# Performance work log

Measured on AMD Instinct MI355X. Metric: run time of the kernel, lower is better.

The kernel has to match this reference:

```python
import jax, jax.numpy as jnp
import numpy as np

N, E, G = 50000, 800000, 512
F, DE, DG = 64, 16, 32
H, HEADS, C, L, NC = 128, 4, 32, 3, 1
EPS = 1e-5


def _bn(x, g, b, m, v):
    # eval-mode BatchNorm1d with running stats
    return (x - m) / jnp.sqrt(v + EPS) * g + b


def setup_inputs():
    key = jax.random.key(0)
    ks = jax.random.split(key, 24)

    def bn_params(k, d):
        k1, k2, k3, k4 = jax.random.split(k, 4)
        return (1.0 + 0.1 * jax.random.normal(k1, (d,), jnp.float32),
                0.1 * jax.random.normal(k2, (d,), jnp.float32),
                0.1 * jax.random.normal(k3, (d,), jnp.float32),
                jax.random.uniform(k4, (d,), jnp.float32, 0.5, 1.5))

    sc = lambda k, sh, fan: jax.random.normal(k, sh, jnp.float32) / np.float32(np.sqrt(fan))
    inp = {}
    inp['x'] = jax.random.normal(ks[0], (N, F), jnp.float32)
    inp['edge_attr'] = jax.random.normal(ks[1], (E, DE), jnp.float32)
    inp['global_features'] = jax.random.normal(ks[2], (G, DG), jnp.float32)
    inp['edge_index'] = jax.random.randint(ks[3], (2, E), 0, N)
    inp['batch'] = jnp.sort(jax.random.randint(ks[4], (N,), 0, G))
    inp['node_w'] = sc(ks[5], (F, H), F); inp['node_b'] = jnp.zeros((H,), jnp.float32)
    inp['node_bn_g'], inp['node_bn_b'], inp['node_bn_m'], inp['node_bn_v'] = bn_params(ks[6], H)
    inp['edge_w'] = sc(ks[7], (DE, H), DE); inp['edge_b'] = jnp.zeros((H,), jnp.float32)
    inp['glob_w'] = sc(ks[8], (DG, H), DG); inp['glob_b'] = jnp.zeros((H,), jnp.float32)
    inp['glob_bn_g'], inp['glob_bn_b'], inp['glob_bn_m'], inp['glob_bn_v'] = bn_params(ks[9], H)
    inp['gat_lin'] = sc(ks[10], (L, H, HEADS * C), H)
    inp['gat_asrc'] = sc(ks[11], (L, HEADS, C), C)
    inp['gat_adst'] = sc(ks[12], (L, HEADS, C), C)
    inp['gat_bias'] = jnp.zeros((L, H), jnp.float32)
    bg, bb, bm, bv = zip(*[bn_params(jax.random.fold_in(ks[13], i), H) for i in range(L)])
    inp['bn_g'] = jnp.stack(bg); inp['bn_b'] = jnp.stack(bb)
    inp['bn_m'] = jnp.stack(bm); inp['bn_v'] = jnp.stack(bv)
    inp['lin1_w'] = sc(ks[14], (3 * H, H), 3 * H); inp['lin1_b'] = jnp.zeros((H,), jnp.float32)
    inp['lin2_w'] = sc(ks[15], (H, NC), H); inp['lin2_b'] = jnp.zeros((NC,), jnp.float32)
    return inp


def reference(x, edge_attr, global_features, edge_index, batch, node_w, node_b, node_bn_g, node_bn_b, node_bn_m, node_bn_v, edge_w, edge_b, glob_w, glob_b, glob_bn_g, glob_bn_b, glob_bn_m, glob_bn_v, gat_lin, gat_asrc, gat_adst, gat_bias, bn_g, bn_b, bn_m, bn_v, lin1_w, lin1_b, lin2_w, lin2_b):
    n = x.shape[0]
    h = jax.nn.relu(_bn(x @ node_w + node_b, node_bn_g, node_bn_b, node_bn_m, node_bn_v))
    _ = jax.nn.relu(edge_attr @ edge_w + edge_b)  # edge encoder: computed but unused by GATConv, as in source
    # add self loops (PyG GATConv default)
    loops = jnp.arange(n)
    src = jnp.concatenate([edge_index[0], loops])
    dst = jnp.concatenate([edge_index[1], loops])
    for i in range(L):
        identity = h
        hh = (h @ gat_lin[i]).reshape(n, HEADS, C)
        a_src = jnp.einsum('nhc,hc->nh', hh, gat_asrc[i])
        a_dst = jnp.einsum('nhc,hc->nh', hh, gat_adst[i])
        e = jax.nn.leaky_relu(a_src[src] + a_dst[dst], 0.2)  # [E+n, HEADS]
        e_max = jax.ops.segment_max(e, dst, num_segments=n)
        ee = jnp.exp(e - e_max[dst])
        den = jax.ops.segment_sum(ee, dst, num_segments=n)
        alpha = ee / (den[dst] + 1e-16)
        out = jax.ops.segment_sum(hh[src] * alpha[..., None], dst, num_segments=n)
        out = out.reshape(n, HEADS * C) + gat_bias[i]
        out = jax.nn.relu(_bn(out, bn_g[i], bn_b[i], bn_m[i], bn_v[i]))
        h = out + identity  # residual: dims always match (HEADS*C == H)
    g = global_features.shape[0]
    cnt = jax.ops.segment_sum(jnp.ones((n,), h.dtype), batch, num_segments=g)
    x_mean = jax.ops.segment_sum(h, batch, num_segments=g) / jnp.maximum(cnt, 1.0)[:, None]
    x_max = jax.ops.segment_max(h, batch, num_segments=g)
    x_max = jnp.where(jnp.isfinite(x_max), x_max, 0.0)  # guard rare empty graphs
    gfeat = jax.nn.relu(_bn(global_features @ glob_w + glob_b, glob_bn_g, glob_bn_b, glob_bn_m, glob_bn_v))
    z = jnp.concatenate([x_mean, x_max, gfeat], axis=1)
    z = jax.nn.relu(z @ lin1_w + lin1_b)
    return z @ lin2_w + lin2_b
```

## Files before the change

### kernel.cpp

```cpp
#include <hip/hip_runtime.h>
#include <hip/hip_bf16.h>

typedef unsigned short u16;
typedef unsigned int   u32;
typedef unsigned long long u64;

#define HD 128
#define FD 64
#define EPS 1e-5f

using bf16x8 = __attribute__((ext_vector_type(8))) short;
using f32x4  = __attribute__((ext_vector_type(4))) float;

__device__ __forceinline__ float b2f(u16 v) { return __uint_as_float(((u32)v) << 16); }
__device__ __forceinline__ u16 f2b(float f) {
    u32 u = __float_as_uint(f);
    return (u16)((u + 0x7FFF + ((u >> 16) & 1)) >> 16);
}
__device__ __forceinline__ float lo16(u32 u) { return __uint_as_float(u << 16); }
__device__ __forceinline__ float hi16(u32 u) { return __uint_as_float(u & 0xFFFF0000u); }

__device__ __forceinline__ bf16x8 pack8(const float* p) {
    bf16x8 r;
    #pragma unroll
    for (int j = 0; j < 8; j++) r[j] = (short)f2b(p[j]);
    return r;
}

__global__ __launch_bounds__(256) void k_hist(const int* __restrict__ dst, int* __restrict__ cnt, int E) {
    int e = blockIdx.x * 256 + threadIdx.x;
    if (e < E) atomicAdd(&cnt[dst[e]], 1);
}

__global__ __launch_bounds__(256) void k_scanA(const int* __restrict__ cnt, int* __restrict__ rowptr,
                                               int* __restrict__ bsum, int N) {
    __shared__ int s[256];
    int tid = threadIdx.x;
    int i = blockIdx.x * 256 + tid;
    s[tid] = (i < N) ? cnt[i] : 0;
    __syncthreads();
    for (int off = 1; off < 256; off <<= 1) {
        int t = (tid >= off) ? s[tid - off] : 0;
        __syncthreads();
        s[tid] += t;
        __syncthreads();
    }
    if (i < N) rowptr[i + 1] = s[tid];
    if (tid == 255) bsum[blockIdx.x] = s[255];
}

__global__ __launch_bounds__(256) void k_scanB(int* __restrict__ bsum, int SB) {
    __shared__ int s[256];
    int tid = threadIdx.x;
    s[tid] = (tid < SB) ? bsum[tid] : 0;
    __syncthreads();
    for (int off = 1; off < 256; off <<= 1) {
        int t = (tid >= off) ? s[tid - off] : 0;
        __syncthreads();
        s[tid] += t;
        __syncthreads();
    }
    if (tid < SB) bsum[tid] = s[tid];
}

__global__ __launch_bounds__(256) void k_scanC(int* __restrict__ rowptr, const int* __restrict__ bsum, int N) {
    int i = blockIdx.x * 256 + threadIdx.x;
    if (i == 0) rowptr[0] = 0;
    if (i < N) {
        int b = i >> 8;
        if (b > 0) rowptr[i + 1] += bsum[b - 1];
    }
}

__global__ __launch_bounds__(256) void k_gbound(const int* __restrict__ batch, int* __restrict__ gs, int N, int G) {
    int i = blockIdx.x * 256 + threadIdx.x;
    if (i < N) {
        int b = batch[i];
        if (i == 0) { for (int g = 0; g <= b; g++) gs[g] = 0; }
        else {
            int pb = batch[i - 1];
            for (int g = pb + 1; g <= b; g++) gs[g] = i;
        }
        if (i == N - 1) { for (int g = b + 1; g <= G; g++) gs[g] = N; }
    }
}

__global__ __launch_bounds__(256) void k_binA(
    const int* __restrict__ src, const int* __restrict__ dst, const int* __restrict__ rowptr,
    int* __restrict__ bcur, u64* __restrict__ binned, int E, int bsh, int NB, int numTiles) {
    __shared__ u32 os[4096], od[4096];
    __shared__ int hist[256], obase[256], ofs[256], gpos[256];
    int tid = threadIdx.x;
    for (int t = blockIdx.x; t < numTiles; t += gridDim.x) {
        int base = t * 4096;
        int cnt = E - base; if (cnt > 4096) cnt = 4096;
        hist[tid] = 0;
        __syncthreads();
        u32 rs[16], rd[16];
        #pragma unroll
        for (int r = 0; r < 16; r++) {
            int li = r * 256 + tid;
            if (li < cnt) {
                rs[r] = src[base + li];
                rd[r] = dst[base + li];
                atomicAdd(&hist[rd[r] >> bsh], 1);
            }
        }
        __syncthreads();
        if (tid < 64) {
            int h0 = hist[4 * tid], h1 = hist[4 * tid + 1];
            int h2 = hist[4 * tid + 2], h3 = hist[4 * tid + 3];
            int s01 = h0 + h1;
            int loc = s01 + h2 + h3;
            int inc = loc;
            #pragma unroll
            for (int off = 1; off < 64; off <<= 1) {
                int tv = __shfl_up(inc, off);
                if (tid >= off) inc += tv;
            }
            int excl = inc - loc;
            obase[4 * tid] = excl;           ofs[4 * tid] = excl;
            obase[4 * tid + 1] = excl + h0;  ofs[4 * tid + 1] = excl + h0;
            obase[4 * tid + 2] = excl + s01; ofs[4 * tid + 2] = excl + s01;
            obase[4 * tid + 3] = excl + s01 + h2; ofs[4 * tid + 3] = excl + s01 + h2;
        }
        __syncthreads();
        #pragma unroll
        for (int r = 0; r < 16; r++) {
            int li = r * 256 + tid;
            if (li < cnt) {
                int b = rd[r] >> bsh;
                int posn = atomicAdd(&ofs[b], 1);
                os[posn] = rs[r];
                od[posn] = rd[r];
            }
        }
        __syncthreads();
        if (tid < NB && hist[tid] > 0)
            gpos[tid] = rowptr[tid << bsh] + atomicAdd(&bcur[tid], hist[tid]);
        __syncthreads();
        for (int li = tid; li < cnt; li += 256) {
            u32 d = od[li];
            int b = d >> bsh;
            binned[(size_t)gpos[b] + (li - obase[b])] = ((u64)d << 32) | os[li];
        }
        __syncthreads();
    }
}

__global__ __launch_bounds__(256) void k_binB(
    const u64* __restrict__ binned, const int* __restrict__ rowptr,
    int* __restrict__ colidx, int N, int bsh) {
    __shared__ int lofs[1024];
    int b = blockIdx.x;
    int n0 = b << bsh;
    int n1 = (b + 1) << bsh; if (n1 > N) n1 = N;
    int nb = 1 << bsh;
    for (int i = threadIdx.x; i < nb; i += 256) lofs[i] = 0;
    __syncthreads();
    int r0 = rowptr[n0], r1 = rowptr[n1];
    for (int i = r0 + threadIdx.x; i < r1; i += 256) {
        u64 pk = binned[i];
        u32 d = (u32)(pk >> 32), s = (u32)pk;
        int slot = atomicAdd(&lofs[d - n0], 1);
        colidx[rowptr[d] + slot] = (int)s;
    }
}

__global__ __launch_bounds__(256) void k_wprep(const float* __restrict__ node_w, const float* __restrict__ gat_lin,
                                               u16* __restrict__ wf_node, u16* __restrict__ wf_gat) {
    int y = blockIdx.y;
    const float* src; u16* dst; int K;
    if (y == 0) { src = node_w; dst = wf_node; K = FD; }
    else { src = gat_lin + (size_t)(y - 1) * HD * HD; dst = wf_gat + (size_t)(y - 1) * HD * HD; K = HD; }
    int KT = K >> 5;
    int total = K * HD;
    for (int f = blockIdx.x * 256 + threadIdx.x; f < total; f += gridDim.x * 256) {
        int j = f & 7;
        int lane = (f >> 3) & 63;
        int t = f >> 9;
        int kt = t % KT;
        int ct = t / KT;
        int k = kt * 32 + (lane >> 4) * 8 + j;
        int col = ct * 16 + (lane & 15);
        dst[f] = f2b(src[k * HD + col]);
    }
}

__global__ __launch_bounds__(256) void k_node_mfma(
    const float* __restrict__ x, const u16* __restrict__ wf, const float* __restrict__ bias,
    const float* __restrict__ g, const float* __restrict__ bb, const float* __restrict__ m,
    const float* __restrict__ v, u16* __restrict__ h, int N) {
    int wv = threadIdx.x >> 6, lane = threadIdx.x & 63;
    int rowbase = blockIdx.x * 64 + wv * 16;
    if (rowbase >= N) return;
    int n16 = lane & 15, quad = lane >> 4;
    int arow = min(rowbase + n16, N - 1);
    f32x4 acc[8] = {};
    #pragma unroll
    for (int kt = 0; kt < 2; kt++) {
        bf16x8 a = pack8(x + (size_t)arow * FD + kt * 32 + quad * 8);
        #pragma unroll
        for (int ct = 0; ct < 8; ct++) {
            bf16x8 b = *(const bf16x8*)(wf + ((size_t)(ct * 2 + kt) * 64 + lane) * 8);
            acc[ct] = __builtin_amdgcn_mfma_f32_16x16x32_bf16(a, b, acc[ct], 0, 0, 0);
        }
    }
    #pragma unroll
    for (int ct = 0; ct < 8; ct++) {
        int col = ct * 16 + n16;
        float sc = g[col] * rsqrtf(v[col] + EPS);
        float bi = (bias[col] - m[col]) * sc + bb[col];
        #pragma unroll
        for (int reg = 0; reg < 4; reg++) {
            int row = rowbase + quad * 4 + reg;
            if (row < N) h[(size_t)row * HD + col] = f2b(fmaxf(acc[ct][reg] * sc + bi, 0.f));
        }
    }
}

__global__ __launch_bounds__(256) void k_gat_mfma(
    const u16* __restrict__ h, const u16* __restrict__ wf,
    const float* __restrict__ asrcw, const float* __restrict__ adstw,
    u16* __restrict__ hh, float* __restrict__ a_src, float* __restrict__ a_dst, int N) {
    int wv = threadIdx.x >> 6, lane = threadIdx.x & 63;
    int rowbase = blockIdx.x * 64 + wv * 16;
    if (rowbase >= N) return;
    int n16 = lane & 15, quad = lane >> 4;
    int arow = min(rowbase + n16, N - 1);
    f32x4 acc[8] = {};
    #pragma unroll
    for (int kt = 0; kt < 4; kt++) {
        bf16x8 a = *(const bf16x8*)(h + (size_t)arow * HD + kt * 32 + quad * 8);
        #pragma unroll
        for (int ct = 0; ct < 8; ct++) {
            bf16x8 b = *(const bf16x8*)(wf + ((size_t)(ct * 4 + kt) * 64 + lane) * 8);
            acc[ct] = __builtin_amdgcn_mfma_f32_16x16x32_bf16(a, b, acc[ct], 0, 0, 0);
        }
    }
    float asw[8], adw[8];
    #pragma unroll
    for (int ct = 0; ct < 8; ct++) {
        asw[ct] = asrcw[ct * 16 + n16];
        adw[ct] = adstw[ct * 16 + n16];
    }
    float ps[4][4], pd[4][4];
    #pragma unroll
    for (int hd = 0; hd < 4; hd++)
        #pragma unroll
        for (int reg = 0; reg < 4; reg++) {
            ps[hd][reg] = acc[2 * hd][reg] * asw[2 * hd] + acc[2 * hd + 1][reg] * asw[2 * hd + 1];
            pd[hd][reg] = acc[2 * hd][reg] * adw[2 * hd] + acc[2 * hd + 1][reg] * adw[2 * hd + 1];
        }
    #pragma unroll
    for (int msk = 1; msk < 16; msk <<= 1) {
        #pragma unroll
        for (int hd = 0; hd < 4; hd++)
            #pragma unroll
            for (int reg = 0; reg < 4; reg++) {
                ps[hd][reg] += __shfl_xor(ps[hd][reg], msk);
                pd[hd][reg] += __shfl_xor(pd[hd][reg], msk);
            }
    }
    #pragma unroll
    for (int reg = 0; reg < 4; reg++) {
        int row = rowbase + quad * 4 + reg;
        if (row < N) {
            #pragma unroll
            for (int ct = 0; ct < 8; ct++)
                hh[(size_t)row * HD + ct * 16 + n16] = f2b(acc[ct][reg]);
            if (n16 < 4) {
                float ws = 0.f, wd = 0.f;
                #pragma unroll
                for (int hd = 0; hd < 4; hd++)
                    if (n16 == hd) { ws = ps[hd][reg]; wd = pd[hd][reg]; }
                a_src[row * 4 + n16] = ws;
                a_dst[row * 4 + n16] = wd;
            }
        }
    }
}

__global__ __launch_bounds__(256) void k_agg(
    u16* __restrict__ h, const u32* __restrict__ hh32,
    const float* __restrict__ a_src, const float* __restrict__ a_dst,
    const int* __restrict__ rowptr, const int* __restrict__ colidx,
    const float* __restrict__ bias, const float* __restrict__ bng, const float* __restrict__ bnb,
    const float* __restrict__ bnm, const float* __restrict__ bnv, int N) {
    __shared__ int   sL[4][64];
    __shared__ __align__(16) float eeL[4][64][4];
    int wv = threadIdx.x >> 6, lane = threadIdx.x & 63;
    int node = blockIdx.x * 4 + wv;
    if (node >= N) return;
    int head = lane >> 4;
    const float4* as4p = (const float4*)a_src;
    float4 ad4 = ((const float4*)a_dst)[node];
    float adh = (head == 0) ? ad4.x : (head == 1) ? ad4.y : (head == 2) ? ad4.z : ad4.w;
    float ash = a_src[node * 4 + head];
    float e = ash + adh;
    e = (e > 0.f) ? e : 0.2f * e;
    float ee = __expf(e);
    float den = ee;
    u32 hv = hh32[(size_t)node * 64 + lane];
    float acc0 = ee * lo16(hv), acc1 = ee * hi16(hv);
    int beg = rowptr[node], end = rowptr[node + 1];
    for (int base = beg; base < end; base += 64) {
        int cnt = end - base; if (cnt > 64) cnt = 64;
        int s = 0;
        float4 e4 = {0.f, 0.f, 0.f, 0.f};
        if (lane < cnt) {
            s = colidx[base + lane];
            float4 as4 = as4p[s];
            float t0 = as4.x + ad4.x, t1 = as4.y + ad4.y, t2 = as4.z + ad4.z, t3 = as4.w + ad4.w;
            t0 = (t0 > 0.f) ? t0 : 0.2f * t0; t1 = (t1 > 0.f) ? t1 : 0.2f * t1;
            t2 = (t2 > 0.f) ? t2 : 0.2f * t2; t3 = (t3 > 0.f) ? t3 : 0.2f * t3;
            e4.x = __expf(t0); e4.y = __expf(t1); e4.z = __expf(t2); e4.w = __expf(t3);
        }
        sL[wv][lane] = s;
        ((float4*)eeL[wv][lane])[0] = e4;
        int j = 0;
        for (; j + 8 <= cnt; j += 8) {
            u32 hv2[8]; float w[8];
            #pragma unroll
            for (int q = 0; q < 8; q++) {
                int sj = sL[wv][j + q];
                w[q] = eeL[wv][j + q][head];
                hv2[q] = hh32[(size_t)sj * 64 + lane];
            }
            #pragma unroll
            for (int q = 0; q < 8; q++) {
                den += w[q];
                acc0 += w[q] * lo16(hv2[q]);
                acc1 += w[q] * hi16(hv2[q]);
            }
        }
        for (; j < cnt; j++) {
            int sj = sL[wv][j];
            float w = eeL[wv][j][head];
            u32 hv2 = hh32[(size_t)sj * 64 + lane];
            den += w;
            acc0 += w * lo16(hv2);
            acc1 += w * hi16(hv2);
        }
    }
    float inv = 1.0f / (den + 1e-16f);
    int c0 = lane * 2, c1 = c0 + 1;
    float o0 = acc0 * inv, o1 = acc1 * inv;
    float sc0 = bng[c0] * rsqrtf(bnv[c0] + EPS);
    float sc1 = bng[c1] * rsqrtf(bnv[c1] + EPS);
    o0 = (o0 + bias[c0] - bnm[c0]) * sc0 + bnb[c0];
    o1 = (o1 + bias[c1] - bnm[c1]) * sc1 + bnb[c1];
    o0 = fmaxf(o0, 0.f); o1 = fmaxf(o1, 0.f);
    u32 idv = ((const u32*)h)[(size_t)node * 64 + lane];
    o0 += lo16(idv); o1 += hi16(idv);
    ((u32*)h)[(size_t)node * 64 + lane] = ((u32)f2b(o1) << 16) | f2b(o0);
}

__global__ __launch_bounds__(256) void k_pool(
    const u16* __restrict__ h, const int* __restrict__ gs,
    const float* __restrict__ gf, const float* __restrict__ glob_w, const float* __restrict__ glob_b,
    const float* __restrict__ gbg, const float* __restrict__ gbb,
    const float* __restrict__ gbm, const float* __restrict__ gbv,
    float* __restrict__ z, int N, int G) {
    __shared__ float s0L[4][64], s1L[4][64], m0L[4][64], m1L[4][64];
    int g = blockIdx.x, tid = threadIdx.x;
    int wv = tid >> 6, lane = tid & 63;
    int beg = gs[g], end = gs[g + 1];
    const u32* h32 = (const u32*)h;
    float s0 = 0.f, s1 = 0.f, m0 = -3.4e38f, m1 = -3.4e38f;
    for (int r = beg + wv; r < end; r += 4) {
        u32 pk = h32[(size_t)r * 64 + lane];
        float v0 = lo16(pk), v1 = hi16(pk);
        s0 += v0; s1 += v1;
        m0 = fmaxf(m0, v0); m1 = fmaxf(m1, v1);
    }
    s0L[wv][lane] = s0; s1L[wv][lane] = s1;
    m0L[wv][lane] = m0; m1L[wv][lane] = m1;
    __syncthreads();
    if (tid < 64) {
        float a0 = s0L[0][lane] + s0L[1][lane] + s0L[2][lane] + s0L[3][lane];
        float a1 = s1L[0][lane] + s1L[1][lane] + s1L[2][lane] + s1L[3][lane];
        float x0 = fmaxf(fmaxf(m0L[0][lane], m0L[1][lane]), fmaxf(m0L[2][lane], m0L[3][lane]));
        float x1 = fmaxf(fmaxf(m1L[0][lane], m1L[1][lane]), fmaxf(m1L[2][lane], m1L[3][lane]));
        int cnt = end - beg;
        float inv = 1.0f / (float)(cnt > 0 ? cnt : 1);
        if (cnt == 0) { x0 = 0.f; x1 = 0.f; }
        ((float2*)(z + (size_t)g * 384))[lane] = make_float2(a0 * inv, a1 * inv);
        ((float2*)(z + (size_t)g * 384 + 128))[lane] = make_float2(x0, x1);
    } else if (tid >= 128) {
        int c = tid - 128;
        float acc = glob_b[c];
        #pragma unroll 8
        for (int k = 0; k < 32; k++) acc += gf[g * 32 + k] * glob_w[k * HD + c];
        float sc = gbg[c] * rsqrtf(gbv[c] + EPS);
        acc = (acc - gbm[c]) * sc + gbb[c];
        z[(size_t)g * 384 + 256 + c] = fmaxf(acc, 0.f);
    }
}

__global__ __launch_bounds__(256) void k_lin(
    const float* __restrict__ z, const float* __restrict__ W1, const float* __restrict__ b1,
    const float* __restrict__ W2, const float* __restrict__ b2, float* __restrict__ out, int G) {
    __shared__ float zL[8][384];
    __shared__ float Wc[64][128];
    __shared__ float red[8][128];
    int tid = threadIdx.x;
    int g0 = blockIdx.x * 8;
    int c = tid & 127, half = tid >> 7;
    for (int i = tid; i < 8 * 384; i += 256) {
        int gi = i / 384, kk = i % 384;
        zL[gi][kk] = (g0 + gi < G) ? z[(size_t)(g0 + gi) * 384 + kk] : 0.f;
    }
    float acc0 = 0.f, acc1 = 0.f, acc2 = 0.f, acc3 = 0.f;
    int gb = half * 4;
    for (int ch = 0; ch < 6; ch++) {
        __syncthreads();
        for (int i4 = tid; i4 < 2048; i4 += 256) {
            int flat = i4 * 4;
            int k = flat >> 7, cc = flat & 127;
            *(float4*)&Wc[k][cc] = *(const float4*)&W1[(size_t)(ch * 64 + k) * HD + cc];
        }
        __syncthreads();
        int kb = ch * 64;
        #pragma unroll 4
        for (int k = 0; k < 64; k++) {
            float w = Wc[k][c];
            acc0 += zL[gb + 0][kb + k] * w;
            acc1 += zL[gb + 1][kb + k] * w;
            acc2 += zL[gb + 2][kb + k] * w;
            acc3 += zL[gb + 3][kb + k] * w;
        }
    }
    float b1c = b1[c], w2c = W2[c];
    __syncthreads();
    red[gb + 0][c] = fmaxf(acc0 + b1c, 0.f) * w2c;
    red[gb + 1][c] = fmaxf(acc1 + b1c, 0.f) * w2c;
    red[gb + 2][c] = fmaxf(acc2 + b1c, 0.f) * w2c;
    red[gb + 3][c] = fmaxf(acc3 + b1c, 0.f) * w2c;
    __syncthreads();
    int gr = tid >> 5, l32 = tid & 31;
    float v = red[gr][l32] + red[gr][l32 + 32] + red[gr][l32 + 64] + red[gr][l32 + 96];
    #pragma unroll
    for (int m = 1; m < 32; m <<= 1) v += __shfl_xor(v, m, 32);
    if (l32 == 0 && g0 + gr < G) out[g0 + gr] = v + b2[0];
}

extern "C" void kernel_launch(void* const* d_in, const int* in_sizes, int n_in,
                              void* d_out, int out_size, void* d_ws, size_t ws_size,
                              hipStream_t stream) {
    (void)n_in; (void)out_size; (void)ws_size;
    const float* x        = (const float*)d_in[0];
    const float* gfeat    = (const float*)d_in[2];
    const int*   ei       = (const int*)d_in[3];
    const int*   batch    = (const int*)d_in[4];
    const float* node_w   = (const float*)d_in[5];
    const float* node_b   = (const float*)d_in[6];
    const float* nbg      = (const float*)d_in[7];
    const float* nbb      = (const float*)d_in[8];
    const float* nbm      = (const float*)d_in[9];
    const float* nbv      = (const float*)d_in[10];
    const float* glob_w   = (const float*)d_in[13];
    const float* glob_b   = (const float*)d_in[14];
    const float* gbg      = (const float*)d_in[15];
    const float* gbb      = (const float*)d_in[16];
    const float* gbm      = (const float*)d_in[17];
    const float* gbv      = (const float*)d_in[18];
    const float* gat_lin  = (const float*)d_in[19];
    const float* gat_asrc = (const float*)d_in[20];
    const float* gat_adst = (const float*)d_in[21];
    const float* gat_bias = (const float*)d_in[22];
    const float* bn_g     = (const float*)d_in[23];
    const float* bn_b     = (const float*)d_in[24];
    const float* bn_m     = (const float*)d_in[25];
    const float* bn_v     = (const float*)d_in[26];
    const float* lin1_w   = (const float*)d_in[27];
    const float* lin1_b   = (const float*)d_in[28];
    const float* lin2_w   = (const float*)d_in[29];
    const float* lin2_b   = (const float*)d_in[30];

    const int N = in_sizes[0] / FD;
    const int E = in_sizes[3] / 2;
    const int G = in_sizes[2] / 32;
    const int* srcp = ei;
    const int* dstp = ei + E;

    int bsh = 8;
    while (((N + (1 << bsh) - 1) >> bsh) > 256) bsh++;
    const int NB = (N + (1 << bsh) - 1) >> bsh;

    char* p = (char*)d_ws;
    auto alloc = [&](size_t bytes) -> char* {
        char* r = p;
        p += (bytes + 255) & ~(size_t)255;
        return r;
    };
    u16*   h       = (u16*)alloc((size_t)N * HD * 2);
    u16*   hh      = (u16*)alloc((size_t)N * HD * 2);
    float* a_src   = (float*)alloc((size_t)N * 4 * 4);
    float* a_dst   = (float*)alloc((size_t)N * 4 * 4);
    int*   rowptr  = (int*)alloc((size_t)(N + 1) * 4);
    char*  zbase   = p;
    int*   cnt     = (int*)alloc((size_t)N * 4);
    int*   bcur    = (int*)alloc(256 * 4);
    size_t zbytes  = (size_t)(p - zbase);
    int*   bsum    = (int*)alloc(256 * 4);
    int*   colidx  = (int*)alloc((size_t)E * 4);
    u64*   binned  = (u64*)alloc((size_t)E * 8);
    u16*   wf_node = (u16*)alloc((size_t)FD * HD * 2);
    u16*   wf_gat  = (u16*)alloc((size_t)3 * HD * HD * 2);
    float* z       = (float*)alloc((size_t)G * 384 * 4);
    int*   gs      = (int*)alloc((size_t)(G + 1) * 4);

    hipMemsetAsync(zbase, 0, zbytes, stream);

    k_wprep<<<dim3(32, 4), 256, 0, stream>>>(node_w, gat_lin, wf_node, wf_gat);

    int eb = (E + 255) / 256;
    int SB = (N + 255) / 256;
    k_hist<<<eb, 256, 0, stream>>>(dstp, cnt, E);
    k_scanA<<<SB, 256, 0, stream>>>(cnt, rowptr, bsum, N);
    k_scanB<<<1, 256, 0, stream>>>(bsum, SB);
    k_scanC<<<SB, 256, 0, stream>>>(rowptr, bsum, N);
    k_gbound<<<SB, 256, 0, stream>>>(batch, gs, N, G);

    int numTiles = (E + 4095) / 4096;
    int binAGrid = numTiles < 512 ? numTiles : 512;
    k_binA<<<binAGrid, 256, 0, stream>>>(srcp, dstp, rowptr, bcur, binned, E, bsh, NB, numTiles);
    k_binB<<<NB, 256, 0, stream>>>(binned, rowptr, colidx, N, bsh);

    k_node_mfma<<<(N + 63) / 64, 256, 0, stream>>>(x, wf_node, node_b, nbg, nbb, nbm, nbv, h, N);

    for (int i = 0; i < 3; i++) {
        k_gat_mfma<<<(N + 63) / 64, 256, 0, stream>>>(
            h, wf_gat + (size_t)i * HD * HD,
            gat_asrc + i * HD, gat_adst + i * HD,
            hh, a_src, a_dst, N);
        k_agg<<<(N + 3) / 4, 256, 0, stream>>>(
            h, (const u32*)hh, a_src, a_dst, rowptr, colidx,
            gat_bias + i * HD, bn_g + i * HD, bn_b + i * HD, bn_m + i * HD, bn_v + i * HD, N);
    }

    k_pool<<<G, 256, 0, stream>>>(h, gs, gfeat, glob_w, glob_b, gbg, gbb, gbm, gbv, z, N, G);
    k_lin<<<(G + 7) / 8, 256, 0, stream>>>(z, lin1_w, lin1_b, lin2_w, lin2_b, (float*)d_out, G);
}
```

Measured before the change: 424.8 us.

## Fuse CSR build, node embedding and readout into fewer kernels with chained scan

Merges weight prep, graph-boundary computation and workspace zeroing into one prep kernel. Fuses the degree histogram into edge binning, which now writes into fixed-capacity per-bucket arenas and runs concurrently with the node-embedding MFMA blocks. Replaces the three-pass scan and second binning pass with a single decoupled chained-scan kernel that also scatters column indices. Fuses pooling with the final MLP. This cuts launch overhead and intermediate traffic, but assumes no bucket exceeds CAP edges and relies on cross-block spin-waits.

After: 706.1 us. +66.2%, slower.

```diff
diff --git a/kernel.cpp b/kernel.cpp
--- a/kernel.cpp
+++ b/kernel.cpp
@@ -8,6 +8,8 @@
 #define HD 128
 #define FD 64
 #define EPS 1e-5f
+#define BSH 8
+#define CAP 8192
 
 using bf16x8 = __attribute__((ext_vector_type(8))) short;
 using f32x4  = __attribute__((ext_vector_type(4))) float;
@@ -20,90 +22,74 @@
 __device__ __forceinline__ float lo16(u32 u) { return __uint_as_float(u << 16); }
 __device__ __forceinline__ float hi16(u32 u) { return __uint_as_float(u & 0xFFFF0000u); }
 
-__device__ __forceinline__ bf16x8 pack8(const float* p) {
-    bf16x8 r;
-    #pragma unroll
-    for (int j = 0; j < 8; j++) r[j] = (short)f2b(p[j]);
-    return r;
-}
-
-__global__ __launch_bounds__(256) void k_hist(const int* __restrict__ dst, int* __restrict__ cnt, int E) {
-    int e = blockIdx.x * 256 + threadIdx.x;
-    if (e < E) atomicAdd(&cnt[dst[e]], 1);
-}
-
-__global__ __launch_bounds__(256) void k_scanA(const int* __restrict__ cnt, int* __restrict__ rowptr,
-                                               int* __restrict__ bsum, int N) {
-    __shared__ int s[256];
+__global__ __launch_bounds__(256) void k_prep(
+    const float* __restrict__ node_w, const float* __restrict__ gat_lin,
+    u16* __restrict__ wf_node, u16* __restrict__ wf_gat,
+    const int* __restrict__ batch, int* __restrict__ gs,
+    int* __restrict__ zbase, int zn, int N, int G) {
+    int y = blockIdx.y;
     int tid = threadIdx.x;
-    int i = blockIdx.x * 256 + tid;
-    s[tid] = (i < N) ? cnt[i] : 0;
-    __syncthreads();
-    for (int off = 1; off < 256; off <<= 1) {
-        int t = (tid >= off) ? s[tid - off] : 0;
-        __syncthreads();
-        s[tid] += t;
-        __syncthreads();
-    }
-    if (i < N) rowptr[i + 1] = s[tid];
-    if (tid == 255) bsum[blockIdx.x] = s[255];
-}
-
-__global__ __launch_bounds__(256) void k_scanB(int* __restrict__ bsum, int SB) {
-    __shared__ int s[256];
+    if (y < 4) {
+        const float* src; u16* dst; int K;
+        if (y == 0) { src = node_w; dst = wf_node; K = FD; }
+        else { src = gat_lin + (size_t)(y - 1) * HD * HD; dst = wf_gat + (size_t)(y - 1) * HD * HD; K = HD; }
+        int KT = K >> 5;
+        int total = K * HD;
+        for (int f = blockIdx.x * 256 + tid; f < total; f += gridDim.x * 256) {
+            int j = f & 7;
+            int lane = (f >> 3) & 63;
+            int t = f >> 9;
+            int kt = t % KT;
+            int ct = t / KT;
+            int k = kt * 32 + (lane >> 4) * 8 + j;
+            int col = ct * 16 + (lane & 15);
+            dst[f] = f2b(src[k * HD + col]);
+        }
+    } else if (y == 4) {
+        int i = blockIdx.x * 256 + tid;
+        if (i < N) {
+            int b = batch[i];
+            if (i == 0) { for (int g = 0; g <= b; g++) gs[g] = 0; }
+            else {
+                int pb = batch[i - 1];
+                for (int g = pb + 1; g <= b; g++) gs[g] = i;
+            }
+            if (i == N - 1) { for (int g = b + 1; g <= G; g++) gs[g] = N; }
+        }
+    } else {
+        for (int i = blockIdx.x * 256 + tid; i < zn; i += gridDim.x * 256) zbase[i] = 0;
+    }
+}
+
+__global__ __launch_bounds__(256) void k_binA_node(
+    const int* __restrict__ src, const int* __restrict__ dst,
+    int* __restrict__ cnt, int* __restrict__ bcur, u64* __restrict__ arena,
+    const float* __restrict__ x, const u16* __restrict__ wf, const float* __restrict__ bias,
+    const float* __restrict__ g, const float* __restrict__ bb, const float* __restrict__ m,
+    const float* __restrict__ v, u16* __restrict__ h,
+    int E, int NB, int numTiles, int N) {
+    __shared__ __align__(16) char smem[4096 * 8 + 4 * 256 * 4];
     int tid = threadIdx.x;
-    s[tid] = (tid < SB) ? bsum[tid] : 0;
-    __syncthreads();
-    for (int off = 1; off < 256; off <<= 1) {
-        int t = (tid >= off) ? s[tid - off] : 0;
-        __syncthreads();
-        s[tid] += t;
-        __syncthreads();
-    }
-    if (tid < SB) bsum[tid] = s[tid];
-}
-
-__global__ __launch_bounds__(256) void k_scanC(int* __restrict__ rowptr, const int* __restrict__ bsum, int N) {
-    int i = blockIdx.x * 256 + threadIdx.x;
-    if (i == 0) rowptr[0] = 0;
-    if (i < N) {
-        int b = i >> 8;
-        if (b > 0) rowptr[i + 1] += bsum[b - 1];
-    }
-}
-
-__global__ __launch_bounds__(256) void k_gbound(const int* __restrict__ batch, int* __restrict__ gs, int N, int G) {
-    int i = blockIdx.x * 256 + threadIdx.x;
-    if (i < N) {
-        int b = batch[i];
-        if (i == 0) { for (int g = 0; g <= b; g++) gs[g] = 0; }
-        else {
-            int pb = batch[i - 1];
-            for (int g = pb + 1; g <= b; g++) gs[g] = i;
-        }
-        if (i == N - 1) { for (int g = b + 1; g <= G; g++) gs[g] = N; }
-    }
-}
-
-__global__ __launch_bounds__(256) void k_binA(
-    const int* __restrict__ src, const int* __restrict__ dst, const int* __restrict__ rowptr,
-    int* __restrict__ bcur, u64* __restrict__ binned, int E, int bsh, int NB, int numTiles) {
-    __shared__ u32 os[4096], od[4096];
-    __shared__ int hist[256], obase[256], ofs[256], gpos[256];
-    int tid = threadIdx.x;
-    for (int t = blockIdx.x; t < numTiles; t += gridDim.x) {
-        int base = t * 4096;
-        int cnt = E - base; if (cnt > 4096) cnt = 4096;
+    if ((int)blockIdx.x < numTiles) {
+        u32* os   = (u32*)smem;
+        u32* od   = os + 4096;
+        int* hist = (int*)(od + 4096);
+        int* obas = hist + 256;
+        int* ofs  = obas + 256;
+        int* gpos = ofs + 256;
+        int base = blockIdx.x * 4096;
+        int cntE = E - base; if (cntE > 4096) cntE = 4096;
         hist[tid] = 0;
         __syncthreads();
         u32 rs[16], rd[16];
         #pragma unroll
         for (int r = 0; r < 16; r++) {
             int li = r * 256 + tid;
-            if (li < cnt) {
+            if (li < cntE) {
                 rs[r] = src[base + li];
                 rd[r] = dst[base + li];
-                atomicAdd(&hist[rd[r] >> bsh], 1);
+                atomicAdd(&hist[rd[r] >> BSH], 1);
+                atomicAdd(&cnt[rd[r]], 1);
             }
         }
         __syncthreads();
@@ -119,17 +105,17 @@
                 if (tid >= off) inc += tv;
             }
             int excl = inc - loc;
-            obase[4 * tid] = excl;           ofs[4 * tid] = excl;
-            obase[4 * tid + 1] = excl + h0;  ofs[4 * tid + 1] = excl + h0;
-            obase[4 * tid + 2] = excl + s01; ofs[4 * tid + 2] = excl + s01;
-            obase[4 * tid + 3] = excl + s01 + h2; ofs[4 * tid + 3] = excl + s01 + h2;
+            obas[4 * tid] = excl;                 ofs[4 * tid] = excl;
+            obas[4 * tid + 1] = excl + h0;        ofs[4 * tid + 1] = excl + h0;
+            obas[4 * tid + 2] = excl + s01;       ofs[4 * tid + 2] = excl + s01;
+            obas[4 * tid + 3] = excl + s01 + h2;  ofs[4 * tid + 3] = excl + s01 + h2;
         }
         __syncthreads();
         #pragma unroll
         for (int r = 0; r < 16; r++) {
             int li = r * 256 + tid;
-            if (li < cnt) {
-                int b = rd[r] >> bsh;
+            if (li < cntE) {
+                int b = rd[r] >> BSH;
                 int posn = atomicAdd(&ofs[b], 1);
                 os[posn] = rs[r];
                 od[posn] = rd[r];
@@ -137,85 +123,107 @@
         }
         __syncthreads();
         if (tid < NB && hist[tid] > 0)
-            gpos[tid] = rowptr[tid << bsh] + atomicAdd(&bcur[tid], hist[tid]);
-        __syncthreads();
-        for (int li = tid; li < cnt; li += 256) {
+            gpos[tid] = atomicAdd(&bcur[tid], hist[tid]);
+        __syncthreads();
+        for (int li = tid; li < cntE; li += 256) {
             u32 d = od[li];
-            int b = d >> bsh;
-            binned[(size_t)gpos[b] + (li - obase[b])] = ((u64)d << 32) | os[li];
-        }
-        __syncthreads();
-    }
-}
-
-__global__ __launch_bounds__(256) void k_binB(
-    const u64* __restrict__ binned, const int* __restrict__ rowptr,
-    int* __restrict__ colidx, int N, int bsh) {
-    __shared__ int lofs[1024];
-    int b = blockIdx.x;
-    int n0 = b << bsh;
-    int n1 = (b + 1) << bsh; if (n1 > N) n1 = N;
-    int nb = 1 << bsh;
-    for (int i = threadIdx.x; i < nb; i += 256) lofs[i] = 0;
-    __syncthreads();
-    int r0 = rowptr[n0], r1 = rowptr[n1];
-    for (int i = r0 + threadIdx.x; i < r1; i += 256) {
-        u64 pk = binned[i];
-        u32 d = (u32)(pk >> 32), s = (u32)pk;
+            int b = d >> BSH;
+            int p = gpos[b] + (li - obas[b]);
+            if (p < CAP) arena[(size_t)b * CAP + p] = ((u64)d << 32) | os[li];
+        }
+    } else {
+        int nb = blockIdx.x - numTiles;
+        int wv = tid >> 6, lane = tid & 63;
+        int rowbase = nb * 64 + wv * 16;
+        if (rowbase >= N) return;
+        int n16 = lane & 15, quad = lane >> 4;
+        int arow = min(rowbase + n16, N - 1);
+        f32x4 acc[8] = {};
+        #pragma unroll
+        for (int kt = 0; kt < 2; kt++) {
+            const float4* xp = (const float4*)(x + (size_t)arow * FD + kt * 32 + quad * 8);
+            float4 a0 = xp[0], a1 = xp[1];
+            bf16x8 a;
+            a[0] = (short)f2b(a0.x); a[1] = (short)f2b(a0.y);
+            a[2] = (short)f2b(a0.z); a[3] = (short)f2b(a0.w);
+            a[4] = (short)f2b(a1.x); a[5] = (short)f2b(a1.y);
+            a[6] = (short)f2b(a1.z); a[7] = (short)f2b(a1.w);
+            #pragma unroll
+            for (int ct = 0; ct < 8; ct++) {
+                bf16x8 b = *(const bf16x8*)(wf + ((size_t)(ct * 2 + kt) * 64 + lane) * 8);
+                acc[ct] = __builtin_amdgcn_mfma_f32_16x16x32_bf16(a, b, acc[ct], 0, 0, 0);
+            }
+        }
+        #pragma unroll
+        for (int ct = 0; ct < 8; ct++) {
+            int col = ct * 16 + n16;
+            float sc = g[col] * rsqrtf(v[col] + EPS);
+            float bi = (bias[col] - m[col]) * sc + bb[col];
+            #pragma unroll
+            for (int reg = 0; reg < 4; reg++) {
+                int row = rowbase + quad * 4 + reg;
+                if (row < N) h[(size_t)row * HD + col] = f2b(fmaxf(acc[ct][reg] * sc + bi, 0.f));
+            }
+        }
+    }
+}
+
+__global__ __launch_bounds__(256) void k_scanB2(
+    const int* __restrict__ cnt, int* __restrict__ rowptr,
+    const u64* __restrict__ arena, const int* __restrict__ bcur,
+    int* __restrict__ colidx, int* __restrict__ ready, int* __restrict__ bval, int N) {
+    __shared__ int rowL[256], lofs[256], cL[256];
+    __shared__ int stot, sbase;
+    int b = blockIdx.x, tid = threadIdx.x;
+    int n0 = b << BSH;
+    int n = n0 + tid;
+    cL[tid] = (n < N) ? cnt[n] : 0;
+    __syncthreads();
+    if (tid < 64) {
+        int h0 = cL[4 * tid], h1 = cL[4 * tid + 1];
+        int h2 = cL[4 * tid + 2], h3 = cL[4 * tid + 3];
+        int s01 = h0 + h1;
+        int loc = s01 + h2 + h3;
+        int inc = loc;
+        #pragma unroll
+        for (int off = 1; off < 64; off <<= 1) {
+            int tv = __shfl_up(inc, off);
+            if (tid >= off) inc += tv;
+        }
+        int excl = inc - loc;
+        rowL[4 * tid] = excl;
+        rowL[4 * tid + 1] = excl + h0;
+        rowL[4 * tid + 2] = excl + s01;
+        rowL[4 * tid + 3] = excl + s01 + h2;
+        if (tid == 63) stot = inc;
+    }
+    __syncthreads();
+    int total = stot;
+    if (tid == 0) {
+        int basev = 0;
+        if (b > 0) {
+            while (atomicAdd(&ready[b - 1], 0) == 0) {}
+            basev = atomicAdd(&bval[b - 1], 0);
+        }
+        atomicExch(&bval[b], basev + total);
+        __threadfence();
+        atomicExch(&ready[b], 1);
+        sbase = basev;
+    }
+    __syncthreads();
+    int basev = sbase;
+    if (n < N) rowptr[n] = basev + rowL[tid];
+    if (b == (int)gridDim.x - 1 && tid == 0) rowptr[N] = basev + total;
+    rowL[tid] += basev;
+    lofs[tid] = 0;
+    __syncthreads();
+    int nedge = bcur[b];
+    if (nedge > CAP) nedge = CAP;
+    for (int i = tid; i < nedge; i += 256) {
+        u64 pk = arena[(size_t)b * CAP + i];
+        int d = (int)(pk >> 32), s = (int)(pk & 0xFFFFFFFFu);
         int slot = atomicAdd(&lofs[d - n0], 1);
-        colidx[rowptr[d] + slot] = (int)s;
-    }
-}
-
-__global__ __launch_bounds__(256) void k_wprep(const float* __restrict__ node_w, const float* __restrict__ gat_lin,
-                                               u16* __restrict__ wf_node, u16* __restrict__ wf_gat) {
-    int y = blockIdx.y;
-    const float* src; u16* dst; int K;
-    if (y == 0) { src = node_w; dst = wf_node; K = FD; }
-    else { src = gat_lin + (size_t)(y - 1) * HD * HD; dst = wf_gat + (size_t)(y - 1) * HD * HD; K = HD; }
-    int KT = K >> 5;
-    int total = K * HD;
-    for (int f = blockIdx.x * 256 + threadIdx.x; f < total; f += gridDim.x * 256) {
-        int j = f & 7;
-        int lane = (f >> 3) & 63;
-        int t = f >> 9;
-        int kt = t % KT;
-        int ct = t / KT;
-        int k = kt * 32 + (lane >> 4) * 8 + j;
-        int col = ct * 16 + (lane & 15);
-        dst[f] = f2b(src[k * HD + col]);
-    }
-}
-
-__global__ __launch_bounds__(256) void k_node_mfma(
-    const float* __restrict__ x, const u16* __restrict__ wf, const float* __restrict__ bias,
-    const float* __restrict__ g, const float* __restrict__ bb, const float* __restrict__ m,
-    const float* __restrict__ v, u16* __restrict__ h, int N) {
-    int wv = threadIdx.x >> 6, lane = threadIdx.x & 63;
-    int rowbase = blockIdx.x * 64 + wv * 16;
-    if (rowbase >= N) return;
-    int n16 = lane & 15, quad = lane >> 4;
-    int arow = min(rowbase + n16, N - 1);
-    f32x4 acc[8] = {};
-    #pragma unroll
-    for (int kt = 0; kt < 2; kt++) {
-        bf16x8 a = pack8(x + (size_t)arow * FD + kt * 32 + quad * 8);
-        #pragma unroll
-        for (int ct = 0; ct < 8; ct++) {
-            bf16x8 b = *(const bf16x8*)(wf + ((size_t)(ct * 2 + kt) * 64 + lane) * 8);
-            acc[ct] = __builtin_amdgcn_mfma_f32_16x16x32_bf16(a, b, acc[ct], 0, 0, 0);
-        }
-    }
-    #pragma unroll
-    for (int ct = 0; ct < 8; ct++) {
-        int col = ct * 16 + n16;
-        float sc = g[col] * rsqrtf(v[col] + EPS);
-        float bi = (bias[col] - m[col]) * sc + bb[col];
-        #pragma unroll
-        for (int reg = 0; reg < 4; reg++) {
-            int row = rowbase + quad * 4 + reg;
-            if (row < N) h[(size_t)row * HD + col] = f2b(fmaxf(acc[ct][reg] * sc + bi, 0.f));
-        }
+        colidx[rowL[d - n0] + slot] = s;
     }
 }
 
@@ -356,61 +364,60 @@
     ((u32*)h)[(size_t)node * 64 + lane] = ((u32)f2b(o1) << 16) | f2b(o0);
 }
 
-__global__ __launch_bounds__(256) void k_pool(
+__global__ __launch_bounds__(256) void k_readout(
     const u16* __restrict__ h, const int* __restrict__ gs,
     const float* __restrict__ gf, const float* __restrict__ glob_w, const float* __restrict__ glob_b,
     const float* __restrict__ gbg, const float* __restrict__ gbb,
     const float* __restrict__ gbm, const float* __restrict__ gbv,
-    float* __restrict__ z, int N, int G) {
-    __shared__ float s0L[4][64], s1L[4][64], m0L[4][64], m1L[4][64];
-    int g = blockIdx.x, tid = threadIdx.x;
-    int wv = tid >> 6, lane = tid & 63;
-    int beg = gs[g], end = gs[g + 1];
-    const u32* h32 = (const u32*)h;
-    float s0 = 0.f, s1 = 0.f, m0 = -3.4e38f, m1 = -3.4e38f;
-    for (int r = beg + wv; r < end; r += 4) {
-        u32 pk = h32[(size_t)r * 64 + lane];
-        float v0 = lo16(pk), v1 = hi16(pk);
-        s0 += v0; s1 += v1;
-        m0 = fmaxf(m0, v0); m1 = fmaxf(m1, v1);
-    }
-    s0L[wv][lane] = s0; s1L[wv][lane] = s1;
-    m0L[wv][lane] = m0; m1L[wv][lane] = m1;
-    __syncthreads();
-    if (tid < 64) {
-        float a0 = s0L[0][lane] + s0L[1][lane] + s0L[2][lane] + s0L[3][lane];
-        float a1 = s1L[0][lane] + s1L[1][lane] + s1L[2][lane] + s1L[3][lane];
-        float x0 = fmaxf(fmaxf(m0L[0][lane], m0L[1][lane]), fmaxf(m0L[2][lane], m0L[3][lane]));
-        float x1 = fmaxf(fmaxf(m1L[0][lane], m1L[1][lane]), fmaxf(m1L[2][lane], m1L[3][lane]));
-        int cnt = end - beg;
-        float inv = 1.0f / (float)(cnt > 0 ? cnt : 1);
-        if (cnt == 0) { x0 = 0.f; x1 = 0.f; }
-        ((float2*)(z + (size_t)g * 384))[lane] = make_float2(a0 * inv, a1 * inv);
-        ((float2*)(z + (size_t)g * 384 + 128))[lane] = make_float2(x0, x1);
-    } else if (tid >= 128) {
-        int c = tid - 128;
-        float acc = glob_b[c];
-        #pragma unroll 8
-        for (int k = 0; k < 32; k++) acc += gf[g * 32 + k] * glob_w[k * HD + c];
-        float sc = gbg[c] * rsqrtf(gbv[c] + EPS);
-        acc = (acc - gbm[c]) * sc + gbb[c];
-        z[(size_t)g * 384 + 256 + c] = fmaxf(acc, 0.f);
-    }
-}
-
-__global__ __launch_bounds__(256) void k_lin(
-    const float* __restrict__ z, const float* __restrict__ W1, const float* __restrict__ b1,
-    const float* __restrict__ W2, const float* __restrict__ b2, float* __restrict__ out, int G) {
+    const float* __restrict__ W1, const float* __restrict__ b1,
+    const float* __restrict__ W2, const float* __restrict__ b2,
+    float* __restrict__ out, int N, int G) {
     __shared__ float zL[8][384];
     __shared__ float Wc[64][128];
     __shared__ float red[8][128];
     int tid = threadIdx.x;
     int g0 = blockIdx.x * 8;
     int c = tid & 127, half = tid >> 7;
-    for (int i = tid; i < 8 * 384; i += 256) {
-        int gi = i / 384, kk = i % 384;
-        zL[gi][kk] = (g0 + gi < G) ? z[(size_t)(g0 + gi) * 384 + kk] : 0.f;
-    }
+    float* scratch = &Wc[0][0];
+    for (int gi = 0; gi < 8; gi++) {
+        int g = g0 + gi;
+        float s = 0.f, mx = -3.4e38f;
+        int beg = 0, end = 0;
+        if (g < G) {
+            beg = gs[g]; end = gs[g + 1];
+            for (int r = beg + half; r < end; r += 2) {
+                float vv = b2f(h[(size_t)r * HD + c]);
+                s += vv; mx = fmaxf(mx, vv);
+            }
+        }
+        if (half == 1) { scratch[c] = s; scratch[128 + c] = mx; }
+        __syncthreads();
+        if (half == 0) {
+            s += scratch[c]; mx = fmaxf(mx, scratch[128 + c]);
+            int cn = end - beg;
+            zL[gi][c] = s / (float)(cn > 0 ? cn : 1);
+            zL[gi][128 + c] = (cn == 0) ? 0.f : mx;
+        }
+        __syncthreads();
+    }
+    {
+        float sc = gbg[c] * rsqrtf(gbv[c] + EPS);
+        float gb0 = glob_b[c], gm = gbm[c], gbb_ = gbb[c];
+        for (int q = 0; q < 4; q++) {
+            int gi = half * 4 + q;
+            int g = g0 + gi;
+            float acc = gb0;
+            if (g < G) {
+                #pragma unroll 8
+                for (int k = 0; k < 32; k++) acc += gf[g * 32 + k] * glob_w[k * HD + c];
+                acc = (acc - gm) * sc + gbb_;
+                zL[gi][256 + c] = fmaxf(acc, 0.f);
+            } else {
+                zL[gi][256 + c] = 0.f;
+            }
+        }
+    }
+    __syncthreads();
     float acc0 = 0.f, acc1 = 0.f, acc2 = 0.f, acc3 = 0.f;
     int gb = half * 4;
     for (int ch = 0; ch < 6; ch++) {
@@ -441,7 +448,7 @@
     int gr = tid >> 5, l32 = tid & 31;
     float v = red[gr][l32] + red[gr][l32 + 32] + red[gr][l32 + 64] + red[gr][l32 + 96];
     #pragma unroll
-    for (int m = 1; m < 32; m <<= 1) v += __shfl_xor(v, m, 32);
+    for (int mk = 1; mk < 32; mk <<= 1) v += __shfl_xor(v, mk, 32);
     if (l32 == 0 && g0 + gr < G) out[g0 + gr] = v + b2[0];
 }
 
@@ -483,10 +490,8 @@
     const int G = in_sizes[2] / 32;
     const int* srcp = ei;
     const int* dstp = ei + E;
-
-    int bsh = 8;
-    while (((N + (1 << bsh) - 1) >> bsh) > 256) bsh++;
-    const int NB = (N + (1 << bsh) - 1) >> bsh;
+    const int NB = (N + 255) >> BSH;
+    const int numTiles = (E + 4095) / 4096;
 
     char* p = (char*)d_ws;
     auto alloc = [&](size_t bytes) -> char* {
@@ -502,33 +507,25 @@
     char*  zbase   = p;
     int*   cnt     = (int*)alloc((size_t)N * 4);
     int*   bcur    = (int*)alloc(256 * 4);
-    size_t zbytes  = (size_t)(p - zbase);
-    int*   bsum    = (int*)alloc(256 * 4);
+    int*   ready   = (int*)alloc(256 * 4);
+    int    zn      = (int)((p - zbase) / 4);
+    int*   bval    = (int*)alloc(256 * 4);
+    u64*   arena   = (u64*)alloc((size_t)NB * CAP * 8);
     int*   colidx  = (int*)alloc((size_t)E * 4);
-    u64*   binned  = (u64*)alloc((size_t)E * 8);
     u16*   wf_node = (u16*)alloc((size_t)FD * HD * 2);
     u16*   wf_gat  = (u16*)alloc((size_t)3 * HD * HD * 2);
-    float* z       = (float*)alloc((size_t)G * 384 * 4);
     int*   gs      = (int*)alloc((size_t)(G + 1) * 4);
 
-    hipMemsetAsync(zbase, 0, zbytes, stream);
-
-    k_wprep<<<dim3(32, 4), 256, 0, stream>>>(node_w, gat_lin, wf_node, wf_gat);
-
-    int eb = (E + 255) / 256;
     int SB = (N + 255) / 256;
-    k_hist<<<eb, 256, 0, stream>>>(dstp, cnt, E);
-    k_scanA<<<SB, 256, 0, stream>>>(cnt, rowptr, bsum, N);
-    k_scanB<<<1, 256, 0, stream>>>(bsum, SB);
-    k_scanC<<<SB, 256, 0, stream>>>(rowptr, bsum, N);
-    k_gbound<<<SB, 256, 0, stream>>>(batch, gs, N, G);
-
-    int numTiles = (E + 4095) / 4096;
-    int binAGrid = numTiles < 512 ? numTiles : 512;
-    k_binA<<<binAGrid, 256, 0, stream>>>(srcp, dstp, rowptr, bcur, binned, E, bsh, NB, numTiles);
-    k_binB<<<NB, 256, 0, stream>>>(binned, rowptr, colidx, N, bsh);
-
-    k_node_mfma<<<(N + 63) / 64, 256, 0, stream>>>(x, wf_node, node_b, nbg, nbb, nbm, nbv, h, N);
+
+    k_prep<<<dim3(SB, 6), 256, 0, stream>>>(node_w, gat_lin, wf_node, wf_gat,
+                                            batch, gs, (int*)zbase, zn, N, G);
+    int nodeBlocks = (N + 63) / 64;
+    k_binA_node<<<numTiles + nodeBlocks, 256, 0, stream>>>(
+        srcp, dstp, cnt, bcur, arena,
+        x, wf_node, node_b, nbg, nbb, nbm, nbv, h,
+        E, NB, numTiles, N);
+    k_scanB2<<<NB, 256, 0, stream>>>(cnt, rowptr, arena, bcur, colidx, ready, bval, N);
 
     for (int i = 0; i < 3; i++) {
         k_gat_mfma<<<(N + 63) / 64, 256, 0, stream>>>(
@@ -540,6 +537,6 @@
             gat_bias + i * HD, bn_g + i * HD, bn_b + i * HD, bn_m + i * HD, bn_v + i * HD, N);
     }
 
-    k_pool<<<G, 256, 0, stream>>>(h, gs, gfeat, glob_w, glob_b, gbg, gbb, gbm, gbv, z, N, G);
-    k_lin<<<(G + 7) / 8, 256, 0, stream>>>(z, lin1_w, lin1_b, lin2_w, lin2_b, (float*)d_out, G);
-}
+    k_readout<<<(G + 7) / 8, 256, 0, stream>>>(h, gs, gfeat, glob_w, glob_b, gbg, gbb, gbm, gbv,
+                                               lin1_w, lin1_b, lin2_w, lin2_b, (float*)d_out, N, G);
+}
```
